# Kernel optimization log

Measured on AMD Instinct MI355X. Metric: run time of the kernel, lower is better.

The kernel has to match this reference:

```python
import jax, jax.numpy as jnp
import numpy as np

DIM = 512
H = 8
HD = DIM // H
B = 1
S = 4096
SCALE = HD ** -0.5


def setup_inputs() -> dict:
    key = jax.random.key(0)
    k1, k2, k3, k4, k5 = jax.random.split(key, 5)
    bound = DIM ** -0.5
    x = jax.random.normal(k1, (B, S, DIM), dtype=jnp.float32)
    q_param = jax.random.uniform(k2, (DIM, H, HD), dtype=jnp.float32, minval=-bound, maxval=bound)
    k_param = jax.random.uniform(k3, (DIM, H, HD), dtype=jnp.float32, minval=-bound, maxval=bound)
    v_param = jax.random.uniform(k4, (DIM, H, HD), dtype=jnp.float32, minval=-bound, maxval=bound)
    p_param = jax.random.uniform(k5, (H, HD, DIM), dtype=jnp.float32, minval=-bound, maxval=bound)
    return {"x": x, "q_param": q_param, "k_param": k_param, "v_param": v_param, "p_param": p_param}


def reference(x, q_param, k_param, v_param, p_param):
    q = jnp.einsum('bsc,chd->bshd', x, q_param) * SCALE
    k = jnp.einsum('btc,chd->bthd', x, k_param)
    v = jnp.einsum('btc,chd->bthd', x, v_param)
    attn = jax.nn.softmax(jnp.einsum('bshd,bthd->bhst', q, k), axis=-1)  # [B,H,S,S]
    o = jnp.einsum('bhst,bthd->bshd', attn, v)
    return jnp.einsum('bshd,hdc->bsc', o, p_param)
```

## Files before the change

### kernel.cpp

```cpp
#include <hip/hip_runtime.h>
#include <hip/hip_bf16.h>
#include <stdint.h>

#define S_LEN 4096
#define DIM   512
#define NH    8
#define HD    64
#define QSCALE 0.18033688011112042f

typedef __attribute__((ext_vector_type(8))) short short8;
typedef __attribute__((ext_vector_type(4))) float f32x4;
typedef __attribute__((ext_vector_type(16))) float f32x16;
typedef __attribute__((ext_vector_type(2))) unsigned uint2v;

__device__ __forceinline__ uint32_t pk2(float lo, float hi) {
  union { __hip_bfloat162 h; uint32_t u; } cv;
  cv.h = __float22bfloat162_rn(float2{lo, hi});
  return cv.u;
}
__device__ __forceinline__ ushort bf1(float x) {
  union { __hip_bfloat16 b; ushort u; } cv;
  cv.b = __float2bfloat16(x);
  return cv.u;
}
__device__ __forceinline__ float bf2f(ushort u) {
  union { uint32_t u; float f; } cv;
  cv.u = (uint32_t)u << 16;
  return cv.f;
}
__device__ __forceinline__ float fexp2(float x) {
  float r;
  asm("v_exp_f32 %0, %1" : "=v"(r) : "v"(x));
  return r;
}

__global__ __launch_bounds__(256)
void cast_x(const float* __restrict__ src, ushort* __restrict__ dst) {
  const int i = (blockIdx.x * 256 + threadIdx.x) * 8;
  const float4 a = *reinterpret_cast<const float4*>(src + i);
  const float4 b = *reinterpret_cast<const float4*>(src + i + 4);
  uint4 o;
  o.x = pk2(a.x, a.y); o.y = pk2(a.z, a.w);
  o.z = pk2(b.x, b.y); o.w = pk2(b.z, b.w);
  *reinterpret_cast<uint4*>(dst + i) = o;
}

__global__ __launch_bounds__(256)
void transpose_w(const float* __restrict__ qp, const float* __restrict__ kp,
                 const float* __restrict__ vp, const float* __restrict__ pp,
                 ushort* __restrict__ wbT, ushort* __restrict__ ppT) {
  __shared__ float L[64][65];
  const int z = blockIdx.z;
  const float* src = (z == 0) ? qp : (z == 1) ? kp : (z == 2) ? vp : pp;
  ushort* dst = (z < 3) ? (wbT + (size_t)z * 512 * 512) : ppT;
  const float scale = (z == 0) ? QSCALE : 1.0f;
  const int k0 = blockIdx.x * 64, n0 = blockIdx.y * 64;
  const int r = threadIdx.x >> 2, c0 = (threadIdx.x & 3) * 16;

#pragma unroll
  for (int j = 0; j < 4; ++j) {
    const float4 v =
        *reinterpret_cast<const float4*>(&src[(k0 + r) * 512 + n0 + c0 + 4 * j]);
    L[r][c0 + 4 * j + 0] = v.x * scale;
    L[r][c0 + 4 * j + 1] = v.y * scale;
    L[r][c0 + 4 * j + 2] = v.z * scale;
    L[r][c0 + 4 * j + 3] = v.w * scale;
  }
  __syncthreads();

  uint4 u0, u1;
  u0.x = pk2(L[c0 + 0][r], L[c0 + 1][r]);
  u0.y = pk2(L[c0 + 2][r], L[c0 + 3][r]);
  u0.z = pk2(L[c0 + 4][r], L[c0 + 5][r]);
  u0.w = pk2(L[c0 + 6][r], L[c0 + 7][r]);
  u1.x = pk2(L[c0 + 8][r], L[c0 + 9][r]);
  u1.y = pk2(L[c0 + 10][r], L[c0 + 11][r]);
  u1.z = pk2(L[c0 + 12][r], L[c0 + 13][r]);
  u1.w = pk2(L[c0 + 14][r], L[c0 + 15][r]);
  ushort* d = dst + (size_t)(n0 + r) * 512 + k0 + c0;
  *reinterpret_cast<uint4*>(d) = u0;
  *reinterpret_cast<uint4*>(d + 8) = u1;
}

template <int MODE>
__global__ __launch_bounds__(256)
void gemm_bf16(const ushort* __restrict__ A, const ushort* __restrict__ Bt,
               void* __restrict__ Cout) {
  __shared__ __align__(16) unsigned char lds[24576];
  const int tid = threadIdx.x;
  const int m0 = blockIdx.x * 128, n0 = blockIdx.y * 64;
  const int lane = tid & 63, w = tid >> 6;
  const int wm = w >> 1, wn = w & 1;
  const int q = lane & 15, g = lane >> 4;
  f32x4 acc[4][2] = {};

  const int ar = tid >> 1, ah = tid & 1;
  const int br = tid >> 2, bq = tid & 3;

  for (int k0 = 0; k0 < 512; k0 += 64) {
    const ushort* ag = A + (size_t)(m0 + ar) * 512 + k0 + ah * 32;
    const uint4 a0 = *reinterpret_cast<const uint4*>(ag);
    const uint4 a1 = *reinterpret_cast<const uint4*>(ag + 8);
    const uint4 a2 = *reinterpret_cast<const uint4*>(ag + 16);
    const uint4 a3 = *reinterpret_cast<const uint4*>(ag + 24);
    const ushort* bg = Bt + (size_t)(n0 + br) * 512 + k0 + bq * 16;
    const uint4 b0 = *reinterpret_cast<const uint4*>(bg);
    const uint4 b1 = *reinterpret_cast<const uint4*>(bg + 8);
    __syncthreads();
    {
      unsigned char* ab = lds + ar * 128;
      const int asw = (ar & 7) << 4;
      *reinterpret_cast<uint4*>(ab + ((ah * 64 + 0) ^ asw)) = a0;
      *reinterpret_cast<uint4*>(ab + ((ah * 64 + 16) ^ asw)) = a1;
      *reinterpret_cast<uint4*>(ab + ((ah * 64 + 32) ^ asw)) = a2;
      *reinterpret_cast<uint4*>(ab + ((ah * 64 + 48) ^ asw)) = a3;
      unsigned char* bb = lds + 16384 + br * 128;
      const int bsw = (br & 7) << 4;
      *reinterpret_cast<uint4*>(bb + ((bq * 32 + 0) ^ bsw)) = b0;
      *reinterpret_cast<uint4*>(bb + ((bq * 32 + 16) ^ bsw)) = b1;
    }
    __syncthreads();

#pragma unroll
    for (int ks = 0; ks < 2; ++ks) {
      short8 bf[2];
#pragma unroll
      for (int ni = 0; ni < 2; ++ni) {
        const int rn = wn * 32 + ni * 16 + q;
        bf[ni] = *reinterpret_cast<const short8*>(
            lds + 16384 + rn * 128 + ((64 * ks + 16 * g) ^ ((rn & 7) << 4)));
      }
#pragma unroll
      for (int mi = 0; mi < 4; ++mi) {
        const int rm = wm * 64 + mi * 16 + q;
        const short8 af = *reinterpret_cast<const short8*>(
            lds + rm * 128 + ((64 * ks + 16 * g) ^ ((rm & 7) << 4)));
#pragma unroll
        for (int ni = 0; ni < 2; ++ni)
          acc[mi][ni] = __builtin_amdgcn_mfma_f32_16x16x32_bf16(
              af, bf[ni], acc[mi][ni], 0, 0, 0);
      }
    }
  }

  if (MODE == 0) {
    ushort* C = (ushort*)Cout;
    const int which = n0 >> 9;
#pragma unroll
    for (int ni = 0; ni < 2; ++ni) {
      const int n = n0 + wn * 32 + ni * 16 + q;
      const int rem = n & 511, hh = rem >> 6, d = rem & 63;
      if (which == 2) {
        ushort* base = C + (size_t)(2 * NH + hh) * (size_t)(S_LEN * HD) +
                       (size_t)d * S_LEN;
#pragma unroll
        for (int mi = 0; mi < 4; ++mi) {
          const int s = m0 + wm * 64 + mi * 16 + 4 * g;
          uint2 pw;
          pw.x = pk2(acc[mi][ni][0], acc[mi][ni][1]);
          pw.y = pk2(acc[mi][ni][2], acc[mi][ni][3]);
          *reinterpret_cast<uint2*>(base + s) = pw;
        }
      } else {
        ushort* base =
            C + ((size_t)which * NH + hh) * (size_t)(S_LEN * HD) + d;
#pragma unroll
        for (int mi = 0; mi < 4; ++mi) {
          const int s = m0 + wm * 64 + mi * 16 + 4 * g;
#pragma unroll
          for (int r = 0; r < 4; ++r)
            base[(size_t)(s + r) * HD] = bf1(acc[mi][ni][r]);
        }
      }
    }
  } else {
    float* C = (float*)Cout;
#pragma unroll
    for (int ni = 0; ni < 2; ++ni) {
      const int n = n0 + wn * 32 + ni * 16 + q;
#pragma unroll
      for (int mi = 0; mi < 4; ++mi) {
        const int s = m0 + wm * 64 + mi * 16 + 4 * g;
#pragma unroll
        for (int r = 0; r < 4; ++r)
          C[(size_t)(s + r) * 512 + n] = acc[mi][ni][r];
      }
    }
  }
}

__global__ __launch_bounds__(256, 2)
void attn_mfma32(const ushort* __restrict__ QKV, ushort* __restrict__ Opart,
                 float2* __restrict__ ML) {
  __shared__ __align__(16) unsigned char lds[32768];
  const int tid = threadIdx.x;
  const int combo = blockIdx.x;
  const int h = combo & 7, z = combo >> 3;
  const int qb = blockIdx.y;
  const int lane = tid & 63, w = tid >> 6;
  const int r31 = lane & 31, hh = lane >> 5;

  const size_t plane = (size_t)S_LEN * HD;
  const ushort* Qp = QKV + (size_t)h * plane;
  const ushort* Kp = QKV + (size_t)(NH + h) * plane;
  const ushort* Vp = QKV + (size_t)(2 * NH + h) * plane;

  const int qbase = qb * 256 + w * 64;
  const int qrowA = qbase + r31, qrowB = qbase + 32 + r31;

  short8 qfA[4], qfB[4];
  {
    const ushort* qa = Qp + (size_t)qrowA * HD + 8 * hh;
    const ushort* qbp = Qp + (size_t)qrowB * HD + 8 * hh;
#pragma unroll
    for (int ks = 0; ks < 4; ++ks) {
      qfA[ks] = *reinterpret_cast<const short8*>(qa + 16 * ks);
      qfB[ks] = *reinterpret_cast<const short8*>(qbp + 16 * ks);
    }
  }

  int roff[4];
#pragma unroll
  for (int ks = 0; ks < 4; ++ks)
    roff[ks] = (((2 * ks + hh) << 4) ^ ((r31 & 7) << 4));
  const int rbase = r31 * 128;

  const int trow = tid >> 2, seg = tid & 3;
  const int tsw = (trow & 7) << 4;
  const int wk0 = trow * 128 + ((seg * 32) ^ tsw);
  const int wk1 = trow * 128 + ((seg * 32 + 16) ^ tsw);
  const ushort* kgbase = Kp + (size_t)(z * 1024 + trow) * HD + seg * 16;
  const ushort* vgbase = Vp + (size_t)trow * S_LEN + z * 1024 + seg * 16;

  f32x16 oA[2] = {}, oB[2] = {};
  float mA = -1e30f, lA = 0.f, mB = -1e30f, lB = 0.f;

  uint4 kst0 = *reinterpret_cast<const uint4*>(kgbase);
  uint4 kst1 = *reinterpret_cast<const uint4*>(kgbase + 8);
  uint4 vst0 = *reinterpret_cast<const uint4*>(vgbase);
  uint4 vst1 = *reinterpret_cast<const uint4*>(vgbase + 8);

  for (int t = 0; t < 16; ++t) {
    const int po = (t & 1) << 14;
    *reinterpret_cast<uint4*>(lds + (wk0 | po)) = kst0;
    *reinterpret_cast<uint4*>(lds + (wk1 | po)) = kst1;
    *reinterpret_cast<uint4*>(lds + ((8192 + wk0) | po)) = vst0;
    *reinterpret_cast<uint4*>(lds + ((8192 + wk1) | po)) = vst1;
    __syncthreads();

    const int tn = (t + 1) & 15;
    kst0 = *reinterpret_cast<const uint4*>(kgbase + tn * 4096);
    kst1 = *reinterpret_cast<const uint4*>(kgbase + tn * 4096 + 8);
    vst0 = *reinterpret_cast<const uint4*>(vgbase + tn * 64);
    vst1 = *reinterpret_cast<const uint4*>(vgbase + tn * 64 + 8);

#pragma unroll
    for (int c = 0; c < 2; ++c) {
      f32x16 sA = {}, sB = {};
#pragma unroll
      for (int ks = 0; ks < 4; ++ks) {
        const short8 af = *reinterpret_cast<const short8*>(
            lds + ((c * 4096 + rbase + roff[ks]) | po));
        sA = __builtin_amdgcn_mfma_f32_32x32x16_bf16(af, qfA[ks], sA, 0, 0, 0);
        sB = __builtin_amdgcn_mfma_f32_32x32x16_bf16(af, qfB[ks], sB, 0, 0, 0);
      }

      {
        float mv[8];
#pragma unroll
        for (int i = 0; i < 8; ++i) mv[i] = fmaxf(sA[i], sA[i + 8]);
#pragma unroll
        for (int i = 0; i < 4; ++i) mv[i] = fmaxf(mv[i], mv[i + 4]);
        float mx = fmaxf(fmaxf(mv[0], mv[1]), fmaxf(mv[2], mv[3]));
        mx = fmaxf(mx, __shfl_xor(mx, 32));
        const bool grow = mx > mA + 8.0f;
        if (__any(grow)) {
          const float mn = grow ? mx : mA;
          const float alpha = grow ? fexp2(mA - mn) : 1.0f;
          lA *= alpha;
#pragma unroll
          for (int i = 0; i < 16; ++i) { oA[0][i] *= alpha; oA[1][i] *= alpha; }
          mA = mn;
        }
        float r0 = 0.f, r1 = 0.f, r2 = 0.f, r3 = 0.f;
#pragma unroll
        for (int i = 0; i < 16; i += 4) {
          sA[i + 0] = fexp2(sA[i + 0] - mA); r0 += sA[i + 0];
          sA[i + 1] = fexp2(sA[i + 1] - mA); r1 += sA[i + 1];
          sA[i + 2] = fexp2(sA[i + 2] - mA); r2 += sA[i + 2];
          sA[i + 3] = fexp2(sA[i + 3] - mA); r3 += sA[i + 3];
        }
        lA += (r0 + r1) + (r2 + r3);
      }
      {
        float mv[8];
#pragma unroll
        for (int i = 0; i < 8; ++i) mv[i] = fmaxf(sB[i], sB[i + 8]);
#pragma unroll
        for (int i = 0; i < 4; ++i) mv[i] = fmaxf(mv[i], mv[i + 4]);
        float mx = fmaxf(fmaxf(mv[0], mv[1]), fmaxf(mv[2], mv[3]));
        mx = fmaxf(mx, __shfl_xor(mx, 32));
        const bool grow = mx > mB + 8.0f;
        if (__any(grow)) {
          const float mn = grow ? mx : mB;
          const float alpha = grow ? fexp2(mB - mn) : 1.0f;
          lB *= alpha;
#pragma unroll
          for (int i = 0; i < 16; ++i) { oB[0][i] *= alpha; oB[1][i] *= alpha; }
          mB = mn;
        }
        float r0 = 0.f, r1 = 0.f, r2 = 0.f, r3 = 0.f;
#pragma unroll
        for (int i = 0; i < 16; i += 4) {
          sB[i + 0] = fexp2(sB[i + 0] - mB); r0 += sB[i + 0];
          sB[i + 1] = fexp2(sB[i + 1] - mB); r1 += sB[i + 1];
          sB[i + 2] = fexp2(sB[i + 2] - mB); r2 += sB[i + 2];
          sB[i + 3] = fexp2(sB[i + 3] - mB); r3 += sB[i + 3];
        }
        lB += (r0 + r1) + (r2 + r3);
      }

      short8 pfA[2], pfB[2];
#pragma unroll
      for (int e = 0; e < 2; ++e) {
        const int bb = 2 * e;
        {
          const uint32_t u00 = pk2(sA[4 * bb + 0], sA[4 * bb + 1]);
          const uint32_t u01 = pk2(sA[4 * bb + 2], sA[4 * bb + 3]);
          const uint32_t u10 = pk2(sA[4 * bb + 4], sA[4 * bb + 5]);
          const uint32_t u11 = pk2(sA[4 * bb + 6], sA[4 * bb + 7]);
          const uint2v se0 =
              __builtin_amdgcn_permlane32_swap(u00, u10, false, false);
          const uint2v se1 =
              __builtin_amdgcn_permlane32_swap(u01, u11, false, false);
          uint32_t fr[4] = {se0.x, se1.x, se0.y, se1.y};
          pfA[e] = *reinterpret_cast<short8*>(fr);
        }
        {
          const uint32_t u00 = pk2(sB[4 * bb + 0], sB[4 * bb + 1]);
          const uint32_t u01 = pk2(sB[4 * bb + 2], sB[4 * bb + 3]);
          const uint32_t u10 = pk2(sB[4 * bb + 4], sB[4 * bb + 5]);
          const uint32_t u11 = pk2(sB[4 * bb + 6], sB[4 * bb + 7]);
          const uint2v se0 =
              __builtin_amdgcn_permlane32_swap(u00, u10, false, false);
          const uint2v se1 =
              __builtin_amdgcn_permlane32_swap(u01, u11, false, false);
          uint32_t fr[4] = {se0.x, se1.x, se0.y, se1.y};
          pfB[e] = *reinterpret_cast<short8*>(fr);
        }
      }

#pragma unroll
      for (int dt = 0; dt < 2; ++dt)
#pragma unroll
        for (int e = 0; e < 2; ++e) {
          const int kg = 2 * c + e;
          const short8 vf = *reinterpret_cast<const short8*>(
              lds + ((8192 + (32 * dt + r31) * 128 +
                      (((32 * kg + 16 * hh)) ^ ((r31 & 7) << 4))) |
                     po));
          oA[dt] = __builtin_amdgcn_mfma_f32_32x32x16_bf16(vf, pfA[e], oA[dt],
                                                           0, 0, 0);
          oB[dt] = __builtin_amdgcn_mfma_f32_32x32x16_bf16(vf, pfB[e], oB[dt],
                                                           0, 0, 0);
        }
    }
  }

  lA += __shfl_xor(lA, 32);
  lB += __shfl_xor(lB, 32);

  if (lane < 32) {
    ML[(size_t)combo * S_LEN + qrowA] = float2{mA, lA};
    ML[(size_t)combo * S_LEN + qrowB] = float2{mB, lB};
  }
  ushort* obA = Opart + ((size_t)combo * S_LEN + qrowA) * HD;
  ushort* obB = Opart + ((size_t)combo * S_LEN + qrowB) * HD;
#pragma unroll
  for (int dt = 0; dt < 2; ++dt)
#pragma unroll
    for (int rq = 0; rq < 4; ++rq) {
      const int d = 32 * dt + 8 * rq + 4 * hh;
      uint2 pwA, pwB;
      pwA.x = pk2(oA[dt][4 * rq + 0], oA[dt][4 * rq + 1]);
      pwA.y = pk2(oA[dt][4 * rq + 2], oA[dt][4 * rq + 3]);
      pwB.x = pk2(oB[dt][4 * rq + 0], oB[dt][4 * rq + 1]);
      pwB.y = pk2(oB[dt][4 * rq + 2], oB[dt][4 * rq + 3]);
      *reinterpret_cast<uint2*>(obA + d) = pwA;
      *reinterpret_cast<uint2*>(obB + d) = pwB;
    }
}

__global__ __launch_bounds__(256)
void combine(const ushort* __restrict__ Opart, const float2* __restrict__ ML,
             ushort* __restrict__ ob) {
  const int t = threadIdx.x;
  const int qq = t & 63, ds = t >> 6;
  const int q = blockIdx.x * 64 + qq;
  const int h = blockIdx.y;

  float m = -1e30f, mz[4], lz[4];
#pragma unroll
  for (int z = 0; z < 4; ++z) {
    const float2 v = ML[(size_t)(z * 8 + h) * S_LEN + q];
    mz[z] = v.x; lz[z] = v.y;
    m = fmaxf(m, v.x);
  }
  float wz[4], l = 0.f;
#pragma unroll
  for (int z = 0; z < 4; ++z) {
    wz[z] = fexp2(mz[z] - m);
    l += wz[z] * lz[z];
  }
  const float inv = 1.0f / l;
#pragma unroll
  for (int z = 0; z < 4; ++z) wz[z] *= inv;

  float acc[16];
#pragma unroll
  for (int i = 0; i < 16; ++i) acc[i] = 0.f;
#pragma unroll
  for (int z = 0; z < 4; ++z) {
    const ushort* src =
        Opart + (((size_t)(z * 8 + h) * S_LEN) + q) * HD + ds * 16;
    const uint4 u0 = *reinterpret_cast<const uint4*>(src);
    const uint4 u1 = *reinterpret_cast<const uint4*>(src + 8);
    const ushort* e0 = reinterpret_cast<const ushort*>(&u0);
    const ushort* e1 = reinterpret_cast<const ushort*>(&u1);
#pragma unroll
    for (int i = 0; i < 8; ++i) {
      acc[i] = fmaf(wz[z], bf2f(e0[i]), acc[i]);
      acc[i + 8] = fmaf(wz[z], bf2f(e1[i]), acc[i + 8]);
    }
  }
  uint32_t pk[8];
#pragma unroll
  for (int i = 0; i < 8; ++i)
    pk[i] = pk2(acc[2 * i], acc[2 * i + 1]);
  ushort* dst = ob + (size_t)q * DIM + h * 64 + ds * 16;
  *reinterpret_cast<uint4*>(dst) = *reinterpret_cast<uint4*>(pk);
  *reinterpret_cast<uint4*>(dst + 8) = *reinterpret_cast<uint4*>(pk + 4);
}

extern "C" void kernel_launch(void* const* d_in, const int* in_sizes, int n_in,
                              void* d_out, int out_size, void* d_ws, size_t ws_size,
                              hipStream_t stream) {
  const float* x  = (const float*)d_in[0];
  const float* qp = (const float*)d_in[1];
  const float* kp = (const float*)d_in[2];
  const float* vp = (const float*)d_in[3];
  const float* pp = (const float*)d_in[4];
  float* out = (float*)d_out;

  unsigned char* ws = (unsigned char*)d_ws;
  ushort* xb    = (ushort*)(ws);
  ushort* qkvb  = (ushort*)(ws + ((size_t)4 << 20));
  ushort* ob    = (ushort*)(ws + ((size_t)16 << 20));
  ushort* wbT   = (ushort*)(ws + ((size_t)20 << 20));
  ushort* ppT   = (ushort*)(ws + ((size_t)22 << 20));
  ushort* opart = (ushort*)(ws + ((size_t)23 << 20));
  float2* ml    = (float2*)(ws + ((size_t)39 << 20));

  cast_x<<<dim3(1024), dim3(256), 0, stream>>>(x, xb);
  transpose_w<<<dim3(8, 8, 4), dim3(256), 0, stream>>>(qp, kp, vp, pp, wbT, ppT);
  gemm_bf16<0><<<dim3(32, 24), dim3(256), 0, stream>>>(xb, wbT, qkvb);
  attn_mfma32<<<dim3(32, 16), dim3(256), 0, stream>>>(qkvb, opart, ml);
  combine<<<dim3(64, 8), dim3(256), 0, stream>>>(opart, ml, ob);
  gemm_bf16<1><<<dim3(32, 8), dim3(256), 0, stream>>>(ob, ppT, out);
}
```

Before: 94.30 us.

## Load K/V MFMA fragments directly from global memory, dropping LDS staging

The attention kernel no longer stages K and V tiles through double-buffered shared memory with block barriers. Each wave now loads its own K and V MFMA operand fragments straight from global memory into registers, with register double-buffering of K across iterations and s_setprio around the MFMA bursts. This removes the LDS writes, the LDS reads and __syncthreads, at the cost of four waves redundantly fetching the same K/V data through the cache and higher register pressure, which may reduce occupancy.

```diff
diff --git a/kernel.cpp b/kernel.cpp
--- a/kernel.cpp
+++ b/kernel.cpp
@@ -190,9 +190,8 @@
 }
 
 __global__ __launch_bounds__(256, 2)
-void attn_mfma32(const ushort* __restrict__ QKV, ushort* __restrict__ Opart,
+void attn_direct(const ushort* __restrict__ QKV, ushort* __restrict__ Opart,
                  float2* __restrict__ ML) {
-  __shared__ __align__(16) unsigned char lds[32768];
   const int tid = threadIdx.x;
   const int combo = blockIdx.x;
   const int h = combo & 7, z = combo >> 3;
@@ -219,50 +218,49 @@
     }
   }
 
-  int roff[4];
-#pragma unroll
-  for (int ks = 0; ks < 4; ++ks)
-    roff[ks] = (((2 * ks + hh) << 4) ^ ((r31 & 7) << 4));
-  const int rbase = r31 * 128;
-
-  const int trow = tid >> 2, seg = tid & 3;
-  const int tsw = (trow & 7) << 4;
-  const int wk0 = trow * 128 + ((seg * 32) ^ tsw);
-  const int wk1 = trow * 128 + ((seg * 32 + 16) ^ tsw);
-  const ushort* kgbase = Kp + (size_t)(z * 1024 + trow) * HD + seg * 16;
-  const ushort* vgbase = Vp + (size_t)trow * S_LEN + z * 1024 + seg * 16;
+  const ushort* kLane = Kp + (size_t)(z * 1024 + r31) * HD + 8 * hh;
+  const ushort* vLane = Vp + (size_t)r31 * S_LEN + z * 1024 + 8 * hh;
 
   f32x16 oA[2] = {}, oB[2] = {};
   float mA = -1e30f, lA = 0.f, mB = -1e30f, lB = 0.f;
 
-  uint4 kst0 = *reinterpret_cast<const uint4*>(kgbase);
-  uint4 kst1 = *reinterpret_cast<const uint4*>(kgbase + 8);
-  uint4 vst0 = *reinterpret_cast<const uint4*>(vgbase);
-  uint4 vst1 = *reinterpret_cast<const uint4*>(vgbase + 8);
-
-  for (int t = 0; t < 16; ++t) {
-    const int po = (t & 1) << 14;
-    *reinterpret_cast<uint4*>(lds + (wk0 | po)) = kst0;
-    *reinterpret_cast<uint4*>(lds + (wk1 | po)) = kst1;
-    *reinterpret_cast<uint4*>(lds + ((8192 + wk0) | po)) = vst0;
-    *reinterpret_cast<uint4*>(lds + ((8192 + wk1) | po)) = vst1;
-    __syncthreads();
-
-    const int tn = (t + 1) & 15;
-    kst0 = *reinterpret_cast<const uint4*>(kgbase + tn * 4096);
-    kst1 = *reinterpret_cast<const uint4*>(kgbase + tn * 4096 + 8);
-    vst0 = *reinterpret_cast<const uint4*>(vgbase + tn * 64);
-    vst1 = *reinterpret_cast<const uint4*>(vgbase + tn * 64 + 8);
+  short8 kfA[8], kfB[8];
+#pragma unroll
+  for (int c = 0; c < 2; ++c)
+#pragma unroll
+    for (int ks = 0; ks < 4; ++ks)
+      kfA[c * 4 + ks] =
+          *reinterpret_cast<const short8*>(kLane + c * 2048 + ks * 16);
+
+  auto body = [&](int t, short8 (&kc)[8], short8 (&kn)[8]) {
+    short8 vf[8];
+#pragma unroll
+    for (int dt = 0; dt < 2; ++dt)
+#pragma unroll
+      for (int kg = 0; kg < 4; ++kg)
+        vf[dt * 4 + kg] = *reinterpret_cast<const short8*>(
+            vLane + dt * 131072 + t * 64 + kg * 16);
 
 #pragma unroll
     for (int c = 0; c < 2; ++c) {
       f32x16 sA = {}, sB = {};
+      __builtin_amdgcn_s_setprio(1);
 #pragma unroll
       for (int ks = 0; ks < 4; ++ks) {
-        const short8 af = *reinterpret_cast<const short8*>(
-            lds + ((c * 4096 + rbase + roff[ks]) | po));
+        const short8 af = kc[c * 4 + ks];
         sA = __builtin_amdgcn_mfma_f32_32x32x16_bf16(af, qfA[ks], sA, 0, 0, 0);
         sB = __builtin_amdgcn_mfma_f32_32x32x16_bf16(af, qfB[ks], sB, 0, 0, 0);
+      }
+      __builtin_amdgcn_s_setprio(0);
+
+      if (c == 0) {
+        const int tn = (t + 1) & 15;
+#pragma unroll
+        for (int cc = 0; cc < 2; ++cc)
+#pragma unroll
+          for (int ks = 0; ks < 4; ++ks)
+            kn[cc * 4 + ks] = *reinterpret_cast<const short8*>(
+                kLane + tn * 4096 + cc * 2048 + ks * 16);
       }
 
       {
@@ -350,21 +348,25 @@
         }
       }
 
+      __builtin_amdgcn_s_setprio(1);
 #pragma unroll
       for (int dt = 0; dt < 2; ++dt)
 #pragma unroll
         for (int e = 0; e < 2; ++e) {
-          const int kg = 2 * c + e;
-          const short8 vf = *reinterpret_cast<const short8*>(
-              lds + ((8192 + (32 * dt + r31) * 128 +
-                      (((32 * kg + 16 * hh)) ^ ((r31 & 7) << 4))) |
-                     po));
-          oA[dt] = __builtin_amdgcn_mfma_f32_32x32x16_bf16(vf, pfA[e], oA[dt],
+          const short8 vfr = vf[dt * 4 + 2 * c + e];
+          oA[dt] = __builtin_amdgcn_mfma_f32_32x32x16_bf16(vfr, pfA[e], oA[dt],
                                                            0, 0, 0);
-          oB[dt] = __builtin_amdgcn_mfma_f32_32x32x16_bf16(vf, pfB[e], oB[dt],
+          oB[dt] = __builtin_amdgcn_mfma_f32_32x32x16_bf16(vfr, pfB[e], oB[dt],
                                                            0, 0, 0);
         }
-    }
+      __builtin_amdgcn_s_setprio(0);
+    }
+  };
+
+#pragma unroll 1
+  for (int tt = 0; tt < 16; tt += 2) {
+    body(tt, kfA, kfB);
+    body(tt + 1, kfB, kfA);
   }
 
   lA += __shfl_xor(lA, 32);
@@ -464,7 +466,7 @@
   cast_x<<<dim3(1024), dim3(256), 0, stream>>>(x, xb);
   transpose_w<<<dim3(8, 8, 4), dim3(256), 0, stream>>>(qp, kp, vp, pp, wbT, ppT);
   gemm_bf16<0><<<dim3(32, 24), dim3(256), 0, stream>>>(xb, wbT, qkvb);
-  attn_mfma32<<<dim3(32, 16), dim3(256), 0, stream>>>(qkvb, opart, ml);
+  attn_direct<<<dim3(32, 16), dim3(256), 0, stream>>>(qkvb, opart, ml);
   combine<<<dim3(64, 8), dim3(256), 0, stream>>>(opart, ml, ob);
   gemm_bf16<1><<<dim3(32, 8), dim3(256), 0, stream>>>(ob, ppT, out);
 }
```

Result: slower. 108.9 us (+15.5%).
